# Kernel optimization log

Measured on AMD Instinct MI355X. Metric: run time of the kernel, lower is better.

## Reference

```python
import jax, jax.numpy as jnp
import numpy as np

N, E, H, IN, C, L, G = 50000, 600000, 128, 128, 4, 3, 128
EPS = 1e-5
BN_SCALE = 1.0 / np.sqrt(1.0 + EPS)  # eval BN with running_mean=0, running_var=1


def _bn(x, g, b):
    return x * (g * BN_SCALE) + b


def _gelu(x):
    return jax.nn.gelu(x, approximate=False)


def setup_inputs() -> dict:
    key = jax.random.key(0)
    ks = jax.random.split(key, 40)
    s = 0.02
    d = {}
    d['x'] = jax.random.normal(ks[0], (N, IN), jnp.float32)
    d['edge_index'] = jax.random.randint(ks[1], (2, E), 0, N)
    d['batch'] = jnp.sort(jax.random.randint(ks[2], (N,), 0, G))
    # input projection
    d['W1'] = jax.random.normal(ks[3], (IN, H)) * s; d['b1'] = jnp.zeros((H,))
    d['g1'] = jnp.ones((H,)); d['be1'] = jnp.zeros((H,))
    d['W2'] = jax.random.normal(ks[4], (H, H)) * s; d['b2'] = jnp.zeros((H,))
    d['g2'] = jnp.ones((H,)); d['be2'] = jnp.zeros((H,))
    # GCN layers (stacked over L)
    d['Wg'] = jax.random.normal(ks[5], (L, H, H)) * s
    d['bg'] = jnp.zeros((L, H))
    d['gg'] = jnp.ones((L, H)); d['bgg'] = jnp.zeros((L, H))
    # graph attention weights
    d['Wa1'] = jax.random.normal(ks[6], (H, H // 2)) * s; d['ba1'] = jnp.zeros((H // 2,))
    d['Wa2'] = jax.random.normal(ks[7], (H // 2, 1)) * s; d['ba2'] = jnp.zeros((1,))
    # classifier
    d['Wc1'] = jax.random.normal(ks[8], (4 * H, 2 * H)) * s; d['bc1'] = jnp.zeros((2 * H,))
    d['gc1'] = jnp.ones((2 * H,)); d['bec1'] = jnp.zeros((2 * H,))
    d['Wc2'] = jax.random.normal(ks[9], (2 * H, H)) * s; d['bc2'] = jnp.zeros((H,))
    d['gc2'] = jnp.ones((H,)); d['bec2'] = jnp.zeros((H,))
    d['Wc3'] = jax.random.normal(ks[10], (H, H // 2)) * s; d['bc3'] = jnp.zeros((H // 2,))
    d['gc3'] = jnp.ones((H // 2,)); d['bec3'] = jnp.zeros((H // 2,))
    d['Wc4'] = jax.random.normal(ks[11], (H // 2, C)) * s; d['bc4'] = jnp.zeros((C,))
    return d


def reference(x, edge_index, batch, W1, b1, g1, be1, W2, b2, g2, be2,
              Wg, bg, gg, bgg, Wa1, ba1, Wa2, ba2,
              Wc1, bc1, gc1, bec1, Wc2, bc2, gc2, bec2,
              Wc3, bc3, gc3, bec3, Wc4, bc4):
    n = x.shape[0]
    src, dst = edge_index[0], edge_index[1]
    # input projection (dropout off in eval)
    h = _gelu(_bn(x @ W1 + b1, g1, be1))
    h = _gelu(_bn(h @ W2 + b2, g2, be2))
    # GCN symmetric norm with self-loops (PyG GCNConv semantics)
    deg = jax.ops.segment_sum(jnp.ones_like(src, dtype=h.dtype), dst, n) + 1.0
    dinv = jax.lax.rsqrt(deg)
    enorm = (dinv[src] * dinv[dst])[:, None]   # [E,1]
    snorm = (dinv * dinv)[:, None]             # [N,1] self-loop weight
    for i in range(L):
        xw = h @ Wg[i]
        agg = jax.ops.segment_sum(xw[src] * enorm, dst, n) + xw * snorm
        h = _gelu(_bn(agg + bg[i], gg[i], bgg[i])) + h
    # attention weights per node
    aw = jnp.tanh(_gelu(h @ Wa1 + ba1) @ Wa2 + ba2)  # [N,1]
    # multi-branch pooling per graph
    cnt = jnp.maximum(jax.ops.segment_sum(jnp.ones((n,), h.dtype), batch, G), 1.0)[:, None]
    x_mean = jax.ops.segment_sum(h, batch, G) / cnt
    x_max = jax.ops.segment_max(h, batch, G)
    x_weighted = jax.ops.segment_sum(h * aw, batch, G) / cnt
    comb = jnp.concatenate([x_mean, x_max, x_mean, x_weighted], axis=-1)  # x_transformer_pooled == x_mean
    z = _gelu(_bn(comb @ Wc1 + bc1, gc1, bec1))
    z = _gelu(_bn(z @ Wc2 + bc2, gc2, bec2))
    z = _gelu(_bn(z @ Wc3 + bc3, gc3, bec3))
    return z @ Wc4 + bc4
```

## Files before the change

### kernel.cpp

```cpp
#include <hip/hip_runtime.h>
#include <hip/hip_bf16.h>
#include <float.h>


#define GGRAPHS 128
#define POOL_NC 16

typedef __attribute__((ext_vector_type(8))) short short8b;
typedef __attribute__((ext_vector_type(4))) float f32x4;

__device__ __forceinline__ float gelu_f(float x) {
    return 0.5f * x * (1.0f + erff(x * 0.7071067811865476f));
}

__device__ __forceinline__ unsigned short f2bf(float f) {
    unsigned int u = __float_as_uint(f);
    unsigned int r = (u + 0x7FFFu + ((u >> 16) & 1u)) >> 16;
    return (unsigned short)r;
}

__device__ __forceinline__ float bf2f(unsigned short u) {
    return __uint_as_float(((unsigned int)u) << 16);
}

static constexpr float BNS_F = 0.99999500003749968f;

__global__ void transpose_all_kernel(const float* __restrict__ W1, const float* __restrict__ W2,
                                     const float* __restrict__ Wg, const float* __restrict__ Wa1,
                                     unsigned short* __restrict__ Wt1, unsigned short* __restrict__ Wt2,
                                     unsigned short* __restrict__ Wtg, unsigned short* __restrict__ Wta1)
{
    const int id = blockIdx.x * 256 + threadIdx.x;
    if (id < 81920) {
        const int m = id >> 14;
        const int r = id & 16383;
        const int k = r >> 7, c = r & 127;
        const float* Wsrc = (m == 0) ? W1 : (m == 1) ? W2 : Wg + (size_t)(m - 2) * 16384;
        unsigned short* Wdst = (m == 0) ? Wt1 : (m == 1) ? Wt2 : Wtg + (size_t)(m - 2) * 16384;
        Wdst[c * 128 + k] = f2bf(Wsrc[r]);
    } else if (id < 90112) {
        const int r = id - 81920;
        const int k = r >> 6, c = r & 63;
        Wta1[c * 128 + k] = f2bf(Wa1[r]);
    }
}

template<int M>
__device__ __forceinline__ void stage_wt(const unsigned short* __restrict__ Wtb,
                                         unsigned short* __restrict__ Wl, int tid)
{
#pragma unroll
    for (int i = 0; i < (M * 16) / 256; ++i) {
        const int idx = i * 256 + tid;
        const uint4 v = reinterpret_cast<const uint4*>(Wtb)[idx];
        const int byte = idx * 16;
        const int swz = byte ^ (((byte >> 8) & 7) << 4);
        *reinterpret_cast<uint4*>(reinterpret_cast<char*>(Wl) + swz) = v;
    }
}

template<int NCT>
__device__ __forceinline__ void mfma_stage(const short8b* a, const unsigned short* __restrict__ Wl,
                                           f32x4* acc, int l4, int lm)
{
    const int swzm = (lm & 7) << 4;
    const char* Wlc = reinterpret_cast<const char*>(Wl);
#pragma unroll
    for (int ks = 0; ks < 4; ++ks) {
#pragma unroll
        for (int ct = 0; ct < NCT; ++ct) {
            const int byte = ct * 4096 + lm * 256 + ks * 64 + l4 * 16;
            const short8b bv = *reinterpret_cast<const short8b*>(Wlc + (byte ^ swzm));
            acc[ct] = __builtin_amdgcn_mfma_f32_16x16x32_bf16(a[ks], bv, acc[ct], 0, 0, 0);
        }
    }
}

__device__ __forceinline__ void load_afrag_bf(const unsigned short* __restrict__ ap, short8b* a)
{
#pragma unroll
    for (int ks = 0; ks < 4; ++ks)
        a[ks] = *reinterpret_cast<const short8b*>(ap + ks * 32);
}

__device__ __forceinline__ void load_afrag_lds(const unsigned short* __restrict__ hl,
                                               int rowl, int l4, short8b* a)
{
    const char* hc = reinterpret_cast<const char*>(hl);
    const int swz = (rowl & 7) << 4;
#pragma unroll
    for (int ks = 0; ks < 4; ++ks) {
        const int byte = rowl * 256 + ks * 64 + l4 * 16;
        a[ks] = *reinterpret_cast<const short8b*>(hc + (byte ^ swz));
    }
}

__device__ __forceinline__ void store_h_lds(unsigned short* __restrict__ hl,
                                            int rowl, int col, unsigned short v)
{
    const int byte = (rowl * 256 + col * 2) ^ ((rowl & 7) << 4);
    *reinterpret_cast<unsigned short*>(reinterpret_cast<char*>(hl) + byte) = v;
}

__global__ __launch_bounds__(256, 2)
void proj_fused(const float* __restrict__ x,
                const unsigned short* __restrict__ Wt1, const unsigned short* __restrict__ Wt2,
                const float* __restrict__ b1, const float* __restrict__ g1, const float* __restrict__ be1,
                const float* __restrict__ b2, const float* __restrict__ g2, const float* __restrict__ be2,
                unsigned short* __restrict__ hbf, int nrows)
{
    __shared__ unsigned short W1l[128 * 128];
    __shared__ unsigned short W2l[128 * 128];
    __shared__ unsigned short h1l[64 * 128];

    const int tid = threadIdx.x;
    stage_wt<128>(Wt1, W1l, tid);
    stage_wt<128>(Wt2, W2l, tid);
    __syncthreads();

    const int w = tid >> 6;
    const int l = tid & 63;
    const int l4 = l >> 4, lm = l & 15;
    const int rowbase = (int)blockIdx.x * 64 + w * 16;

    int arow = rowbase + lm; if (arow >= nrows) arow = nrows - 1;
    const float* apf = x + (size_t)arow * 128 + l4 * 8;
    short8b a[4];
#pragma unroll
    for (int ks = 0; ks < 4; ++ks) {
        const float4 v0 = *reinterpret_cast<const float4*>(apf + ks * 32);
        const float4 v1 = *reinterpret_cast<const float4*>(apf + ks * 32 + 4);
        short8b av;
        av[0] = (short)f2bf(v0.x); av[1] = (short)f2bf(v0.y);
        av[2] = (short)f2bf(v0.z); av[3] = (short)f2bf(v0.w);
        av[4] = (short)f2bf(v1.x); av[5] = (short)f2bf(v1.y);
        av[6] = (short)f2bf(v1.z); av[7] = (short)f2bf(v1.w);
        a[ks] = av;
    }

    f32x4 acc[8];
#pragma unroll
    for (int ct = 0; ct < 8; ++ct) acc[ct] = f32x4{0.f, 0.f, 0.f, 0.f};
    mfma_stage<8>(a, W1l, acc, l4, lm);

#pragma unroll
    for (int ct = 0; ct < 8; ++ct) {
        const int col = ct * 16 + lm;
        const float g = g1[col];
        const float sc = g * BNS_F;
        const float bi = b1[col] * sc + be1[col];
#pragma unroll
        for (int rid = 0; rid < 4; ++rid) {
            const int rowl = w * 16 + l4 * 4 + rid;
            float v = acc[ct][rid] * sc + bi;
            v = gelu_f(v);
            store_h_lds(h1l, rowl, col, f2bf(v));
        }
    }
    __syncthreads();

    load_afrag_lds(h1l, w * 16 + lm, l4, a);
#pragma unroll
    for (int ct = 0; ct < 8; ++ct) acc[ct] = f32x4{0.f, 0.f, 0.f, 0.f};
    mfma_stage<8>(a, W2l, acc, l4, lm);

#pragma unroll
    for (int ct = 0; ct < 8; ++ct) {
        const int col = ct * 16 + lm;
        const float g = g2[col];
        const float sc = g * BNS_F;
        const float bi = b2[col] * sc + be2[col];
#pragma unroll
        for (int rid = 0; rid < 4; ++rid) {
            const int row = rowbase + l4 * 4 + rid;
            if (row < nrows) {
                float v = acc[ct][rid] * sc + bi;
                v = gelu_f(v);
                hbf[(size_t)row * 128 + col] = f2bf(v);
            }
        }
    }
}

__global__ __launch_bounds__(256, 2)
void gemm_gcn(const unsigned short* __restrict__ Abf,
              const unsigned short* __restrict__ Wtb,
              const float* __restrict__ bias, const float* __restrict__ gam,
              const float* __restrict__ beta, unsigned short* __restrict__ hbf,
              int nrows)
{
    __shared__ unsigned short Wl[128 * 128];

    const int tid = threadIdx.x;
    stage_wt<128>(Wtb, Wl, tid);
    __syncthreads();

    const int w = tid >> 6;
    const int l = tid & 63;
    const int l4 = l >> 4, lm = l & 15;
    const int rowbase = (int)blockIdx.x * 64 + w * 16;

    int arow = rowbase + lm; if (arow >= nrows) arow = nrows - 1;
    short8b a[4];
    load_afrag_bf(Abf + (size_t)arow * 128 + l4 * 8, a);

    f32x4 acc[8];
#pragma unroll
    for (int ct = 0; ct < 8; ++ct) acc[ct] = f32x4{0.f, 0.f, 0.f, 0.f};
    mfma_stage<8>(a, Wl, acc, l4, lm);

#pragma unroll
    for (int ct = 0; ct < 8; ++ct) {
        const int col = ct * 16 + lm;
        const float g = gam[col];
        const float sc = g * BNS_F;
        const float bi = bias[col] * sc + beta[col];
#pragma unroll
        for (int rid = 0; rid < 4; ++rid) {
            const int row = rowbase + l4 * 4 + rid;
            if (row < nrows) {
                float v = acc[ct][rid] * sc + bi;
                v = gelu_f(v);
                v += bf2f(hbf[(size_t)row * 128 + col]);
                hbf[(size_t)row * 128 + col] = f2bf(v);
            }
        }
    }
}

__global__ __launch_bounds__(256, 2)
void gcn_aw_fused(const unsigned short* __restrict__ Abf,
                  const unsigned short* __restrict__ Wt3,
                  const float* __restrict__ bias, const float* __restrict__ gam,
                  const float* __restrict__ beta, unsigned short* __restrict__ hbf,
                  const unsigned short* __restrict__ Wta1, const float* __restrict__ ba1,
                  const float* __restrict__ Wa2, const float* __restrict__ ba2,
                  float* __restrict__ awout, int nrows)
{
    __shared__ unsigned short W3l[128 * 128];
    __shared__ unsigned short Wa1l[64 * 128];
    __shared__ unsigned short hl[64 * 128];

    const int tid = threadIdx.x;
    stage_wt<128>(Wt3, W3l, tid);
    stage_wt<64>(Wta1, Wa1l, tid);
    __syncthreads();

    const int w = tid >> 6;
    const int l = tid & 63;
    const int l4 = l >> 4, lm = l & 15;
    const int rowbase = (int)blockIdx.x * 64 + w * 16;

    int arow = rowbase + lm; if (arow >= nrows) arow = nrows - 1;
    short8b a[4];
    load_afrag_bf(Abf + (size_t)arow * 128 + l4 * 8, a);

    f32x4 acc[8];
#pragma unroll
    for (int ct = 0; ct < 8; ++ct) acc[ct] = f32x4{0.f, 0.f, 0.f, 0.f};
    mfma_stage<8>(a, W3l, acc, l4, lm);

#pragma unroll
    for (int ct = 0; ct < 8; ++ct) {
        const int col = ct * 16 + lm;
        const float g = gam[col];
        const float sc = g * BNS_F;
        const float bi = bias[col] * sc + beta[col];
#pragma unroll
        for (int rid = 0; rid < 4; ++rid) {
            const int row = rowbase + l4 * 4 + rid;
            const int rowl = w * 16 + l4 * 4 + rid;
            float v = acc[ct][rid] * sc + bi;
            v = gelu_f(v);
            unsigned short hv;
            if (row < nrows) {
                v += bf2f(hbf[(size_t)row * 128 + col]);
                hv = f2bf(v);
                hbf[(size_t)row * 128 + col] = hv;
            } else {
                hv = 0;
            }
            store_h_lds(hl, rowl, col, hv);
        }
    }
    __syncthreads();

    load_afrag_lds(hl, w * 16 + lm, l4, a);
    f32x4 acc2[4];
#pragma unroll
    for (int ct = 0; ct < 4; ++ct) acc2[ct] = f32x4{0.f, 0.f, 0.f, 0.f};
    mfma_stage<4>(a, Wa1l, acc2, l4, lm);

    float p[4] = {0.f, 0.f, 0.f, 0.f};
#pragma unroll
    for (int ct = 0; ct < 4; ++ct) {
        const int col = ct * 16 + lm;
        const float bi = ba1[col];
        const float wa = Wa2[col];
#pragma unroll
        for (int rid = 0; rid < 4; ++rid) {
            float v = acc2[ct][rid] + bi;
            v = gelu_f(v);
            p[rid] = fmaf(v, wa, p[rid]);
        }
    }
    const float ba2v = ba2[0];
#pragma unroll
    for (int rid = 0; rid < 4; ++rid) {
        float v = p[rid];
        v += __shfl_xor(v, 1);
        v += __shfl_xor(v, 2);
        v += __shfl_xor(v, 4);
        v += __shfl_xor(v, 8);
        const int row = rowbase + l4 * 4 + rid;
        if (lm == 0 && row < nrows) awout[row] = tanhf(v + ba2v);
    }
}

__global__ void count_rank_kernel(const int* __restrict__ dst, int* __restrict__ cnt,
                                  int* __restrict__ rank, int E)
{
    int e = blockIdx.x * 256 + threadIdx.x;
    if (e < E) rank[e] = atomicAdd(&cnt[dst[e]], 1);
}

__global__ void scan_local(const int* __restrict__ cnt, int* __restrict__ rowptr,
                           int* __restrict__ bsum, float* __restrict__ dinv, int n)
{
    __shared__ int sd[1024];
    const int tid = threadIdx.x;
    const int i = blockIdx.x * 1024 + tid;
    int v = (i < n) ? cnt[i] : 0;
    if (i < n) dinv[i] = rsqrtf((float)v + 1.0f);
    sd[tid] = v;
    __syncthreads();
    for (int off = 1; off < 1024; off <<= 1) {
        int t = (tid >= off) ? sd[tid - off] : 0;
        __syncthreads();
        sd[tid] += t;
        __syncthreads();
    }
    if (i < n) rowptr[i + 1] = sd[tid];
    if (tid == 1023) bsum[blockIdx.x] = sd[1023];
}

__global__ void scan_add(int* __restrict__ rowptr, const int* __restrict__ bsum, int n)
{
    __shared__ int pref;
    const int bid = blockIdx.x;
    if (threadIdx.x < 64) {
        int v = ((int)threadIdx.x < bid) ? bsum[threadIdx.x] : 0;
#pragma unroll
        for (int off = 32; off; off >>= 1) v += __shfl_xor(v, off);
        if (threadIdx.x == 0) pref = v;
    }
    __syncthreads();
    const int i = bid * 1024 + threadIdx.x;
    if (i < n) rowptr[i + 1] += pref;
    if (i == 0) rowptr[0] = 0;
}

__global__ void fill_kernel(const int* __restrict__ src, const int* __restrict__ dst,
                            const float* __restrict__ dinv, const int* __restrict__ rowptr,
                            const int* __restrict__ rank, int2* __restrict__ csr, int E)
{
    int e = blockIdx.x * 256 + threadIdx.x;
    if (e < E) {
        const int d = dst[e], s = src[e];
        const int pos = rowptr[d] + rank[e];
        int2 p;
        p.x = s;
        p.y = __float_as_int(dinv[s] * dinv[d]);
        csr[pos] = p;
    }
}

#define FMAB(A, Wt, U) { A.x = fmaf(Wt, bf2f(U.x), A.x); A.y = fmaf(Wt, bf2f(U.y), A.y); \
                         A.z = fmaf(Wt, bf2f(U.z), A.z); A.w = fmaf(Wt, bf2f(U.w), A.w); }

__global__ __launch_bounds__(256)
void agg_kernel(const ushort4* __restrict__ hb, const int2* __restrict__ csr,
                const int* __restrict__ rowptr, const float* __restrict__ dinv,
                ushort4* __restrict__ ahb, int n)
{
    const int node = blockIdx.x * 8 + (threadIdx.x >> 5);
    if (node >= n) return;
    const int lane = threadIdx.x & 31;

    const float di = dinv[node];
    const float sw = di * di;
    const ushort4 sv = hb[(size_t)node * 32 + lane];
    float4 a0, a1;
    a0.x = bf2f(sv.x) * sw; a0.y = bf2f(sv.y) * sw;
    a0.z = bf2f(sv.z) * sw; a0.w = bf2f(sv.w) * sw;
    a1.x = 0.f; a1.y = 0.f; a1.z = 0.f; a1.w = 0.f;

    const int beg = rowptr[node], end = rowptr[node + 1];
    int s = beg;
    for (; s + 4 <= end; s += 4) {
        const int2 e0 = csr[s+0], e1 = csr[s+1], e2 = csr[s+2], e3 = csr[s+3];
        const ushort4 v0 = hb[(size_t)e0.x * 32 + lane];
        const ushort4 v1 = hb[(size_t)e1.x * 32 + lane];
        const ushort4 v2 = hb[(size_t)e2.x * 32 + lane];
        const ushort4 v3 = hb[(size_t)e3.x * 32 + lane];
        FMAB(a0, __int_as_float(e0.y), v0); FMAB(a1, __int_as_float(e1.y), v1);
        FMAB(a0, __int_as_float(e2.y), v2); FMAB(a1, __int_as_float(e3.y), v3);
    }
    for (; s < end; ++s) {
        const int2 e0 = csr[s];
        const ushort4 v = hb[(size_t)e0.x * 32 + lane];
        FMAB(a0, __int_as_float(e0.y), v);
    }
    ushort4 q;
    q.x = f2bf(a0.x + a1.x); q.y = f2bf(a0.y + a1.y);
    q.z = f2bf(a0.z + a1.z); q.w = f2bf(a0.w + a1.w);
    ahb[(size_t)node * 32 + lane] = q;
}

__device__ __forceinline__ int lb_batch(const int* __restrict__ batch, int n, int t)
{
    int lo = 0, hi = n;
    while (lo < hi) { int mid = (lo + hi) >> 1; if (batch[mid] < t) lo = mid + 1; else hi = mid; }
    return lo;
}

__global__ void pool_partial(const unsigned short* __restrict__ h, const float* __restrict__ aw,
                             const int* __restrict__ batch, int n, float* __restrict__ ps,
                             float* __restrict__ pm, float* __restrict__ pw)
{
    const int g = blockIdx.x >> 4;
    const int c = blockIdx.x & (POOL_NC - 1);
    const int f = threadIdx.x;
    const int beg = lb_batch(batch, n, g), end = lb_batch(batch, n, g + 1);
    const int len = end - beg;
    const int cbeg = beg + (int)(((long long)len * c) / POOL_NC);
    const int cend = beg + (int)(((long long)len * (c + 1)) / POOL_NC);
    float s = 0.f, m = -FLT_MAX, w = 0.f;
    for (int node = cbeg; node < cend; ++node) {
        const float v = bf2f(h[(size_t)node * 128 + f]);
        const float a = aw[node];
        s += v;
        m = fmaxf(m, v);
        w = fmaf(v, a, w);
    }
    const size_t idx = ((size_t)g * POOL_NC + c) * 128 + f;
    ps[idx] = s; pm[idx] = m; pw[idx] = w;
}

__global__ void pool_final(const float* __restrict__ ps, const float* __restrict__ pm,
                           const float* __restrict__ pw, const int* __restrict__ batch,
                           int n, float* __restrict__ comb)
{
    const int g = blockIdx.x;
    const int f = threadIdx.x;
    float s = 0.f, m = -FLT_MAX, w = 0.f;
#pragma unroll
    for (int c = 0; c < POOL_NC; ++c) {
        const size_t idx = ((size_t)g * POOL_NC + c) * 128 + f;
        s += ps[idx];
        m = fmaxf(m, pm[idx]);
        w += pw[idx];
    }
    float cn = (float)(lb_batch(batch, n, g + 1) - lb_batch(batch, n, g));
    if (cn < 1.f) cn = 1.f;
    comb[(size_t)g * 512 + f]       = s / cn;
    comb[(size_t)g * 512 + 128 + f] = m;
    comb[(size_t)g * 512 + 256 + f] = s / cn;
    comb[(size_t)g * 512 + 384 + f] = w / cn;
}

template<int K, int M, bool DO_BN, bool DO_GELU>
__global__ __launch_bounds__(256)
void rowgemm2(const float* __restrict__ X, const float* __restrict__ W,
              const float* __restrict__ bias, const float* __restrict__ gam,
              const float* __restrict__ beta, float* __restrict__ Y)
{
    constexpr int NC = M / 64;
    constexpr int KQ = K / 4;
    const int row = blockIdx.x / NC;
    const int lane = threadIdx.x & 63;
    const int c = (blockIdx.x % NC) * 64 + lane;
    const int q = threadIdx.x >> 6;

    const float* __restrict__ xq = X + (size_t)row * K + q * KQ;
    const float* __restrict__ wq = W + (size_t)(q * KQ) * M + c;

    float a0 = 0.f, a1 = 0.f, a2 = 0.f, a3 = 0.f;
#pragma unroll 4
    for (int k = 0; k < KQ; k += 4) {
        const float4 xv = *reinterpret_cast<const float4*>(xq + k);
        a0 = fmaf(xv.x, wq[(size_t)(k + 0) * M], a0);
        a1 = fmaf(xv.y, wq[(size_t)(k + 1) * M], a1);
        a2 = fmaf(xv.z, wq[(size_t)(k + 2) * M], a2);
        a3 = fmaf(xv.w, wq[(size_t)(k + 3) * M], a3);
    }
    __shared__ float part[4][64];
    part[q][lane] = (a0 + a1) + (a2 + a3);
    __syncthreads();
    if (q == 0) {
        float v = (part[0][lane] + part[1][lane]) + (part[2][lane] + part[3][lane]);
        if (DO_BN) { const float g = gam[c]; const float sc = g * BNS_F; v = v * sc + (bias[c] * sc + beta[c]); }
        else       { v = v + bias[c]; }
        if (DO_GELU) v = gelu_f(v);
        Y[(size_t)row * M + c] = v;
    }
}

__global__ void rowgemm_final(const float* __restrict__ X, const float* __restrict__ W,
                              const float* __restrict__ bias, float* __restrict__ Y)
{
    const int row = blockIdx.x;
    const int lane = threadIdx.x;
    const float xv = X[(size_t)row * 64 + lane];
    const float4 wr = *reinterpret_cast<const float4*>(W + lane * 4);
    float a0 = xv * wr.x, a1 = xv * wr.y, a2 = xv * wr.z, a3 = xv * wr.w;
#pragma unroll
    for (int off = 32; off; off >>= 1) {
        a0 += __shfl_xor(a0, off);
        a1 += __shfl_xor(a1, off);
        a2 += __shfl_xor(a2, off);
        a3 += __shfl_xor(a3, off);
    }
    if (lane == 0) {
        Y[(size_t)row * 4 + 0] = a0 + bias[0];
        Y[(size_t)row * 4 + 1] = a1 + bias[1];
        Y[(size_t)row * 4 + 2] = a2 + bias[2];
        Y[(size_t)row * 4 + 3] = a3 + bias[3];
    }
}

extern "C" void kernel_launch(void* const* d_in, const int* in_sizes, int n_in,
                              void* d_out, int out_size, void* d_ws, size_t ws_size,
                              hipStream_t stream)
{
    const float* x     = (const float*)d_in[0];
    const int*   ei    = (const int*)d_in[1];
    const int*   batch = (const int*)d_in[2];
    const float* W1  = (const float*)d_in[3];
    const float* b1  = (const float*)d_in[4];
    const float* g1  = (const float*)d_in[5];
    const float* be1 = (const float*)d_in[6];
    const float* W2  = (const float*)d_in[7];
    const float* b2  = (const float*)d_in[8];
    const float* g2  = (const float*)d_in[9];
    const float* be2 = (const float*)d_in[10];
    const float* Wg  = (const float*)d_in[11];
    const float* bg  = (const float*)d_in[12];
    const float* gg  = (const float*)d_in[13];
    const float* bgg = (const float*)d_in[14];
    const float* Wa1 = (const float*)d_in[15];
    const float* ba1 = (const float*)d_in[16];
    const float* Wa2 = (const float*)d_in[17];
    const float* ba2 = (const float*)d_in[18];
    const float* Wc1 = (const float*)d_in[19];
    const float* bc1 = (const float*)d_in[20];
    const float* gc1 = (const float*)d_in[21];
    const float* bec1= (const float*)d_in[22];
    const float* Wc2 = (const float*)d_in[23];
    const float* bc2 = (const float*)d_in[24];
    const float* gc2 = (const float*)d_in[25];
    const float* bec2= (const float*)d_in[26];
    const float* Wc3 = (const float*)d_in[27];
    const float* bc3 = (const float*)d_in[28];
    const float* gc3 = (const float*)d_in[29];
    const float* bec3= (const float*)d_in[30];
    const float* Wc4 = (const float*)d_in[31];
    const float* bc4 = (const float*)d_in[32];
    float* out = (float*)d_out;

    const int N = in_sizes[0] / 128;
    const int E = in_sizes[1] / 2;
    const int G = GGRAPHS;

    size_t off = 0;
    auto alloc = [&](size_t bytes) -> void* {
        void* p = (char*)d_ws + off;
        off += (bytes + 255) & ~(size_t)255;
        return p;
    };
    unsigned short* hbf   = (unsigned short*)alloc((size_t)N * 128 * 2);
    unsigned short* ahb   = (unsigned short*)alloc((size_t)N * 128 * 2);
    unsigned short* Wt1   = (unsigned short*)alloc(128 * 128 * 2);
    unsigned short* Wt2   = (unsigned short*)alloc(128 * 128 * 2);
    unsigned short* Wtg   = (unsigned short*)alloc(3 * 128 * 128 * 2);
    unsigned short* Wta1  = (unsigned short*)alloc(64 * 128 * 2);
    float*   aw     = (float*)alloc((size_t)N * 4);
    float*   dinv   = (float*)alloc((size_t)N * 4);
    int*     cnt    = (int*)alloc((size_t)N * 4);
    int*     rank   = (int*)alloc((size_t)E * 4);
    int*     rowptr = (int*)alloc((size_t)(N + 1) * 4);
    int*     bsum   = (int*)alloc(64 * 4);
    int2*    csr    = (int2*)alloc((size_t)E * 8);
    float*   comb   = (float*)alloc((size_t)G * 512 * 4);
    float*   ps     = (float*)alloc((size_t)G * POOL_NC * 128 * 4);
    float*   pm     = (float*)alloc((size_t)G * POOL_NC * 128 * 4);
    float*   pw     = (float*)alloc((size_t)G * POOL_NC * 128 * 4);
    float*   z1     = (float*)alloc((size_t)G * 256 * 4);
    float*   z2     = (float*)alloc((size_t)G * 128 * 4);
    float*   z3     = (float*)alloc((size_t)G * 64 * 4);
    (void)ws_size;

    const int* e_src = ei;
    const int* e_dst = ei + E;

    transpose_all_kernel<<<352, 256, 0, stream>>>(W1, W2, Wg, Wa1, Wt1, Wt2, Wtg, Wta1);

    hipMemsetAsync(cnt, 0, (size_t)N * 4, stream);
    count_rank_kernel<<<(E + 255) / 256, 256, 0, stream>>>(e_dst, cnt, rank, E);
    const int nb = (N + 1023) / 1024;
    scan_local<<<nb, 1024, 0, stream>>>(cnt, rowptr, bsum, dinv, N);
    scan_add<<<nb, 1024, 0, stream>>>(rowptr, bsum, N);
    fill_kernel<<<(E + 255) / 256, 256, 0, stream>>>(e_src, e_dst, dinv, rowptr, rank, csr, E);

    const int rowblocks = (N + 63) / 64;

    proj_fused<<<rowblocks, 256, 0, stream>>>(
        x, Wt1, Wt2, b1, g1, be1, b2, g2, be2, hbf, N);

    for (int l = 0; l < 2; ++l) {
        agg_kernel<<<(N + 7) / 8, 256, 0, stream>>>(
            (const ushort4*)hbf, csr, rowptr, dinv, (ushort4*)ahb, N);
        gemm_gcn<<<rowblocks, 256, 0, stream>>>(
            ahb, Wtg + (size_t)l * 16384, bg + (size_t)l * 128,
            gg + (size_t)l * 128, bgg + (size_t)l * 128, hbf, N);
    }

    agg_kernel<<<(N + 7) / 8, 256, 0, stream>>>(
        (const ushort4*)hbf, csr, rowptr, dinv, (ushort4*)ahb, N);
    gcn_aw_fused<<<rowblocks, 256, 0, stream>>>(
        ahb, Wtg + (size_t)2 * 16384, bg + (size_t)2 * 128,
        gg + (size_t)2 * 128, bgg + (size_t)2 * 128, hbf,
        Wta1, ba1, Wa2, ba2, aw, N);

    pool_partial<<<G * POOL_NC, 128, 0, stream>>>(hbf, aw, batch, N, ps, pm, pw);
    pool_final<<<G, 128, 0, stream>>>(ps, pm, pw, batch, N, comb);

    rowgemm2<512, 256, true, true><<<G * 4, 256, 0, stream>>>(comb, Wc1, bc1, gc1, bec1, z1);
    rowgemm2<256, 128, true, true><<<G * 2, 256, 0, stream>>>(z1, Wc2, bc2, gc2, bec2, z2);
    rowgemm2<128, 64,  true, true><<<G * 1, 256, 0, stream>>>(z2, Wc3, bc3, gc3, bec3, z3);
    rowgemm_final<<<G, 64, 0, stream>>>(z3, Wc4, bc4, out);
}
```

Measured before the change: 386.7 us.

## Read MFMA weights from global memory and fuse pooling-final plus classifier head

The GEMM kernels no longer stage transposed bf16 weights into LDS. Each lane now loads its B fragments straight from global memory, where they should hit in L1/L2, which removes the per-block staging cost and the barrier and raises occupancy by freeing LDS. Separately, pool_final and the four classifier GEMM launches are merged into one head_kernel per graph that keeps the intermediates in shared memory, removing four launches and their global round trips. The risks are more redundant global weight loads per MFMA inside the hot loops, and less parallelism in the head, since each block computes all 256 Wc1 columns alone.

After: 436.5 us. 1.13x slower.

```diff
diff --git a/kernel.cpp b/kernel.cpp
--- a/kernel.cpp
+++ b/kernel.cpp
@@ -45,32 +45,16 @@
     }
 }
 
-template<int M>
-__device__ __forceinline__ void stage_wt(const unsigned short* __restrict__ Wtb,
-                                         unsigned short* __restrict__ Wl, int tid)
-{
-#pragma unroll
-    for (int i = 0; i < (M * 16) / 256; ++i) {
-        const int idx = i * 256 + tid;
-        const uint4 v = reinterpret_cast<const uint4*>(Wtb)[idx];
-        const int byte = idx * 16;
-        const int swz = byte ^ (((byte >> 8) & 7) << 4);
-        *reinterpret_cast<uint4*>(reinterpret_cast<char*>(Wl) + swz) = v;
-    }
-}
-
 template<int NCT>
-__device__ __forceinline__ void mfma_stage(const short8b* a, const unsigned short* __restrict__ Wl,
-                                           f32x4* acc, int l4, int lm)
-{
-    const int swzm = (lm & 7) << 4;
-    const char* Wlc = reinterpret_cast<const char*>(Wl);
+__device__ __forceinline__ void mfma_global(const short8b* a, const unsigned short* __restrict__ Wtb,
+                                            f32x4* acc, int l4, int lm)
+{
 #pragma unroll
     for (int ks = 0; ks < 4; ++ks) {
 #pragma unroll
         for (int ct = 0; ct < NCT; ++ct) {
-            const int byte = ct * 4096 + lm * 256 + ks * 64 + l4 * 16;
-            const short8b bv = *reinterpret_cast<const short8b*>(Wlc + (byte ^ swzm));
+            const short8b bv = *reinterpret_cast<const short8b*>(
+                Wtb + (size_t)(ct * 16 + lm) * 128 + ks * 32 + l4 * 8);
             acc[ct] = __builtin_amdgcn_mfma_f32_16x16x32_bf16(a[ks], bv, acc[ct], 0, 0, 0);
         }
     }
@@ -109,15 +93,9 @@
                 const float* __restrict__ b2, const float* __restrict__ g2, const float* __restrict__ be2,
                 unsigned short* __restrict__ hbf, int nrows)
 {
-    __shared__ unsigned short W1l[128 * 128];
-    __shared__ unsigned short W2l[128 * 128];
     __shared__ unsigned short h1l[64 * 128];
 
     const int tid = threadIdx.x;
-    stage_wt<128>(Wt1, W1l, tid);
-    stage_wt<128>(Wt2, W2l, tid);
-    __syncthreads();
-
     const int w = tid >> 6;
     const int l = tid & 63;
     const int l4 = l >> 4, lm = l & 15;
@@ -141,7 +119,7 @@
     f32x4 acc[8];
 #pragma unroll
     for (int ct = 0; ct < 8; ++ct) acc[ct] = f32x4{0.f, 0.f, 0.f, 0.f};
-    mfma_stage<8>(a, W1l, acc, l4, lm);
+    mfma_global<8>(a, Wt1, acc, l4, lm);
 
 #pragma unroll
     for (int ct = 0; ct < 8; ++ct) {
@@ -162,7 +140,7 @@
     load_afrag_lds(h1l, w * 16 + lm, l4, a);
 #pragma unroll
     for (int ct = 0; ct < 8; ++ct) acc[ct] = f32x4{0.f, 0.f, 0.f, 0.f};
-    mfma_stage<8>(a, W2l, acc, l4, lm);
+    mfma_global<8>(a, Wt2, acc, l4, lm);
 
 #pragma unroll
     for (int ct = 0; ct < 8; ++ct) {
@@ -189,12 +167,7 @@
               const float* __restrict__ beta, unsigned short* __restrict__ hbf,
               int nrows)
 {
-    __shared__ unsigned short Wl[128 * 128];
-
     const int tid = threadIdx.x;
-    stage_wt<128>(Wtb, Wl, tid);
-    __syncthreads();
-
     const int w = tid >> 6;
     const int l = tid & 63;
     const int l4 = l >> 4, lm = l & 15;
@@ -207,7 +180,7 @@
     f32x4 acc[8];
 #pragma unroll
     for (int ct = 0; ct < 8; ++ct) acc[ct] = f32x4{0.f, 0.f, 0.f, 0.f};
-    mfma_stage<8>(a, Wl, acc, l4, lm);
+    mfma_global<8>(a, Wtb, acc, l4, lm);
 
 #pragma unroll
     for (int ct = 0; ct < 8; ++ct) {
@@ -237,15 +210,9 @@
                   const float* __restrict__ Wa2, const float* __restrict__ ba2,
                   float* __restrict__ awout, int nrows)
 {
-    __shared__ unsigned short W3l[128 * 128];
-    __shared__ unsigned short Wa1l[64 * 128];
     __shared__ unsigned short hl[64 * 128];
 
     const int tid = threadIdx.x;
-    stage_wt<128>(Wt3, W3l, tid);
-    stage_wt<64>(Wta1, Wa1l, tid);
-    __syncthreads();
-
     const int w = tid >> 6;
     const int l = tid & 63;
     const int l4 = l >> 4, lm = l & 15;
@@ -258,7 +225,7 @@
     f32x4 acc[8];
 #pragma unroll
     for (int ct = 0; ct < 8; ++ct) acc[ct] = f32x4{0.f, 0.f, 0.f, 0.f};
-    mfma_stage<8>(a, W3l, acc, l4, lm);
+    mfma_global<8>(a, Wt3, acc, l4, lm);
 
 #pragma unroll
     for (int ct = 0; ct < 8; ++ct) {
@@ -289,7 +256,7 @@
     f32x4 acc2[4];
 #pragma unroll
     for (int ct = 0; ct < 4; ++ct) acc2[ct] = f32x4{0.f, 0.f, 0.f, 0.f};
-    mfma_stage<4>(a, Wa1l, acc2, l4, lm);
+    mfma_global<4>(a, Wta1, acc2, l4, lm);
 
     float p[4] = {0.f, 0.f, 0.f, 0.f};
 #pragma unroll
@@ -447,85 +414,115 @@
     ps[idx] = s; pm[idx] = m; pw[idx] = w;
 }
 
-__global__ void pool_final(const float* __restrict__ ps, const float* __restrict__ pm,
-                           const float* __restrict__ pw, const int* __restrict__ batch,
-                           int n, float* __restrict__ comb)
-{
+__global__ __launch_bounds__(256)
+void head_kernel(const float* __restrict__ ps, const float* __restrict__ pm,
+                 const float* __restrict__ pw, const int* __restrict__ batch, int n,
+                 const float* __restrict__ Wc1, const float* __restrict__ bc1,
+                 const float* __restrict__ gc1, const float* __restrict__ bec1,
+                 const float* __restrict__ Wc2, const float* __restrict__ bc2,
+                 const float* __restrict__ gc2, const float* __restrict__ bec2,
+                 const float* __restrict__ Wc3, const float* __restrict__ bc3,
+                 const float* __restrict__ gc3, const float* __restrict__ bec3,
+                 const float* __restrict__ Wc4, const float* __restrict__ bc4,
+                 float* __restrict__ out)
+{
+    __shared__ float comb[512];
+    __shared__ float z1[256];
+    __shared__ float z2[128];
+    __shared__ float z3[64];
+
     const int g = blockIdx.x;
-    const int f = threadIdx.x;
-    float s = 0.f, m = -FLT_MAX, w = 0.f;
-#pragma unroll
-    for (int c = 0; c < POOL_NC; ++c) {
-        const size_t idx = ((size_t)g * POOL_NC + c) * 128 + f;
-        s += ps[idx];
-        m = fmaxf(m, pm[idx]);
-        w += pw[idx];
-    }
-    float cn = (float)(lb_batch(batch, n, g + 1) - lb_batch(batch, n, g));
-    if (cn < 1.f) cn = 1.f;
-    comb[(size_t)g * 512 + f]       = s / cn;
-    comb[(size_t)g * 512 + 128 + f] = m;
-    comb[(size_t)g * 512 + 256 + f] = s / cn;
-    comb[(size_t)g * 512 + 384 + f] = w / cn;
-}
-
-template<int K, int M, bool DO_BN, bool DO_GELU>
-__global__ __launch_bounds__(256)
-void rowgemm2(const float* __restrict__ X, const float* __restrict__ W,
-              const float* __restrict__ bias, const float* __restrict__ gam,
-              const float* __restrict__ beta, float* __restrict__ Y)
-{
-    constexpr int NC = M / 64;
-    constexpr int KQ = K / 4;
-    const int row = blockIdx.x / NC;
-    const int lane = threadIdx.x & 63;
-    const int c = (blockIdx.x % NC) * 64 + lane;
-    const int q = threadIdx.x >> 6;
-
-    const float* __restrict__ xq = X + (size_t)row * K + q * KQ;
-    const float* __restrict__ wq = W + (size_t)(q * KQ) * M + c;
-
-    float a0 = 0.f, a1 = 0.f, a2 = 0.f, a3 = 0.f;
+    const int tid = threadIdx.x;
+
+    if (tid < 128) {
+        float s = 0.f, m = -FLT_MAX, w = 0.f;
+#pragma unroll
+        for (int c = 0; c < POOL_NC; ++c) {
+            const size_t idx = ((size_t)g * POOL_NC + c) * 128 + tid;
+            s += ps[idx];
+            m = fmaxf(m, pm[idx]);
+            w += pw[idx];
+        }
+        float cn = (float)(lb_batch(batch, n, g + 1) - lb_batch(batch, n, g));
+        if (cn < 1.f) cn = 1.f;
+        comb[tid]       = s / cn;
+        comb[128 + tid] = m;
+        comb[256 + tid] = s / cn;
+        comb[384 + tid] = w / cn;
+    }
+    __syncthreads();
+
+    {
+        const int c = tid;
+        float a0 = 0.f, a1 = 0.f, a2 = 0.f, a3 = 0.f;
 #pragma unroll 4
-    for (int k = 0; k < KQ; k += 4) {
-        const float4 xv = *reinterpret_cast<const float4*>(xq + k);
-        a0 = fmaf(xv.x, wq[(size_t)(k + 0) * M], a0);
-        a1 = fmaf(xv.y, wq[(size_t)(k + 1) * M], a1);
-        a2 = fmaf(xv.z, wq[(size_t)(k + 2) * M], a2);
-        a3 = fmaf(xv.w, wq[(size_t)(k + 3) * M], a3);
-    }
-    __shared__ float part[4][64];
-    part[q][lane] = (a0 + a1) + (a2 + a3);
-    __syncthreads();
-    if (q == 0) {
-        float v = (part[0][lane] + part[1][lane]) + (part[2][lane] + part[3][lane]);
-        if (DO_BN) { const float g = gam[c]; const float sc = g * BNS_F; v = v * sc + (bias[c] * sc + beta[c]); }
-        else       { v = v + bias[c]; }
-        if (DO_GELU) v = gelu_f(v);
-        Y[(size_t)row * M + c] = v;
-    }
-}
-
-__global__ void rowgemm_final(const float* __restrict__ X, const float* __restrict__ W,
-                              const float* __restrict__ bias, float* __restrict__ Y)
-{
-    const int row = blockIdx.x;
-    const int lane = threadIdx.x;
-    const float xv = X[(size_t)row * 64 + lane];
-    const float4 wr = *reinterpret_cast<const float4*>(W + lane * 4);
-    float a0 = xv * wr.x, a1 = xv * wr.y, a2 = xv * wr.z, a3 = xv * wr.w;
-#pragma unroll
-    for (int off = 32; off; off >>= 1) {
-        a0 += __shfl_xor(a0, off);
-        a1 += __shfl_xor(a1, off);
-        a2 += __shfl_xor(a2, off);
-        a3 += __shfl_xor(a3, off);
-    }
-    if (lane == 0) {
-        Y[(size_t)row * 4 + 0] = a0 + bias[0];
-        Y[(size_t)row * 4 + 1] = a1 + bias[1];
-        Y[(size_t)row * 4 + 2] = a2 + bias[2];
-        Y[(size_t)row * 4 + 3] = a3 + bias[3];
+        for (int k = 0; k < 512; k += 4) {
+            const float4 xv = *reinterpret_cast<const float4*>(&comb[k]);
+            a0 = fmaf(xv.x, Wc1[(size_t)(k + 0) * 256 + c], a0);
+            a1 = fmaf(xv.y, Wc1[(size_t)(k + 1) * 256 + c], a1);
+            a2 = fmaf(xv.z, Wc1[(size_t)(k + 2) * 256 + c], a2);
+            a3 = fmaf(xv.w, Wc1[(size_t)(k + 3) * 256 + c], a3);
+        }
+        float v = (a0 + a1) + (a2 + a3);
+        const float sc = gc1[c] * BNS_F;
+        v = v * sc + (bc1[c] * sc + bec1[c]);
+        z1[c] = gelu_f(v);
+    }
+    __syncthreads();
+
+    if (tid < 128) {
+        const int c = tid;
+        float a0 = 0.f, a1 = 0.f, a2 = 0.f, a3 = 0.f;
+#pragma unroll 4
+        for (int k = 0; k < 256; k += 4) {
+            const float4 xv = *reinterpret_cast<const float4*>(&z1[k]);
+            a0 = fmaf(xv.x, Wc2[(size_t)(k + 0) * 128 + c], a0);
+            a1 = fmaf(xv.y, Wc2[(size_t)(k + 1) * 128 + c], a1);
+            a2 = fmaf(xv.z, Wc2[(size_t)(k + 2) * 128 + c], a2);
+            a3 = fmaf(xv.w, Wc2[(size_t)(k + 3) * 128 + c], a3);
+        }
+        float v = (a0 + a1) + (a2 + a3);
+        const float sc = gc2[c] * BNS_F;
+        v = v * sc + (bc2[c] * sc + bec2[c]);
+        z2[c] = gelu_f(v);
+    }
+    __syncthreads();
+
+    if (tid < 64) {
+        const int c = tid;
+        float a0 = 0.f, a1 = 0.f, a2 = 0.f, a3 = 0.f;
+#pragma unroll 4
+        for (int k = 0; k < 128; k += 4) {
+            const float4 xv = *reinterpret_cast<const float4*>(&z2[k]);
+            a0 = fmaf(xv.x, Wc3[(size_t)(k + 0) * 64 + c], a0);
+            a1 = fmaf(xv.y, Wc3[(size_t)(k + 1) * 64 + c], a1);
+            a2 = fmaf(xv.z, Wc3[(size_t)(k + 2) * 64 + c], a2);
+            a3 = fmaf(xv.w, Wc3[(size_t)(k + 3) * 64 + c], a3);
+        }
+        float v = (a0 + a1) + (a2 + a3);
+        const float sc = gc3[c] * BNS_F;
+        v = v * sc + (bc3[c] * sc + bec3[c]);
+        z3[c] = gelu_f(v);
+    }
+    __syncthreads();
+
+    if (tid < 64) {
+        const float xv = z3[tid];
+        const float4 wr = *reinterpret_cast<const float4*>(Wc4 + tid * 4);
+        float a0 = xv * wr.x, a1 = xv * wr.y, a2 = xv * wr.z, a3 = xv * wr.w;
+#pragma unroll
+        for (int off = 32; off; off >>= 1) {
+            a0 += __shfl_xor(a0, off);
+            a1 += __shfl_xor(a1, off);
+            a2 += __shfl_xor(a2, off);
+            a3 += __shfl_xor(a3, off);
+        }
+        if (tid == 0) {
+            out[(size_t)g * 4 + 0] = a0 + bc4[0];
+            out[(size_t)g * 4 + 1] = a1 + bc4[1];
+            out[(size_t)g * 4 + 2] = a2 + bc4[2];
+            out[(size_t)g * 4 + 3] = a3 + bc4[3];
+        }
     }
 }
 
@@ -591,13 +588,9 @@
     int*     rowptr = (int*)alloc((size_t)(N + 1) * 4);
     int*     bsum   = (int*)alloc(64 * 4);
     int2*    csr    = (int2*)alloc((size_t)E * 8);
-    float*   comb   = (float*)alloc((size_t)G * 512 * 4);
     float*   ps     = (float*)alloc((size_t)G * POOL_NC * 128 * 4);
     float*   pm     = (float*)alloc((size_t)G * POOL_NC * 128 * 4);
     float*   pw     = (float*)alloc((size_t)G * POOL_NC * 128 * 4);
-    float*   z1     = (float*)alloc((size_t)G * 256 * 4);
-    float*   z2     = (float*)alloc((size_t)G * 128 * 4);
-    float*   z3     = (float*)alloc((size_t)G * 64 * 4);
     (void)ws_size;
 
     const int* e_src = ei;
@@ -633,10 +626,8 @@
         Wta1, ba1, Wa2, ba2, aw, N);
 
     pool_partial<<<G * POOL_NC, 128, 0, stream>>>(hbf, aw, batch, N, ps, pm, pw);
-    pool_final<<<G, 128, 0, stream>>>(ps, pm, pw, batch, N, comb);
-
-    rowgemm2<512, 256, true, true><<<G * 4, 256, 0, stream>>>(comb, Wc1, bc1, gc1, bec1, z1);
-    rowgemm2<256, 128, true, true><<<G * 2, 256, 0, stream>>>(z1, Wc2, bc2, gc2, bec2, z2);
-    rowgemm2<128, 64,  true, true><<<G * 1, 256, 0, stream>>>(z2, Wc3, bc3, gc3, bec3, z3);
-    rowgemm_final<<<G, 64, 0, stream>>>(z3, Wc4, bc4, out);
-}
+
+    head_kernel<<<G, 256, 0, stream>>>(ps, pm, pw, batch, N,
+                                       Wc1, bc1, gc1, bec1, Wc2, bc2, gc2, bec2,
+                                       Wc3, bc3, gc3, bec3, Wc4, bc4, out);
+}
```
